# Kernel tuning notes

Hardware: AMD Instinct MI355X
Metric: run time of the kernel (lower is better)

## Reference

```python
import jax, jax.numpy as jnp
import numpy as np

N_RAYS = 65536
N_COARSE = 64
N_FINE = 128


def setup_inputs() -> dict:
    key = jax.random.key(0)
    k0, k1, k2 = jax.random.split(key, 3)
    origins = jax.random.normal(k0, (N_RAYS, 3), dtype=jnp.float32)
    directions = jax.random.normal(k1, (N_RAYS, 3), dtype=jnp.float32)
    near = jnp.full((N_RAYS,), 2.0, dtype=jnp.float32)
    far = jnp.full((N_RAYS,), 6.0, dtype=jnp.float32)
    # coarse-pass weights used for inverse-CDF (PDF) fine sampling
    weights = jax.random.uniform(k2, (N_RAYS, N_COARSE), dtype=jnp.float32)
    return {"origins": origins, "directions": directions, "near": near,
            "far": far, "weights": weights}


def sample_pdf(bins, weights, n_samples):
    """Inverse-CDF sampling. bins: [N, B], weights: [N, B-1] -> [N, n_samples]."""
    w = weights + 1e-5                       # avoid nans / empty bins
    pdf = w / jnp.sum(w, axis=-1, keepdims=True)
    cdf = jnp.cumsum(pdf, axis=-1)
    cdf = jnp.concatenate([jnp.zeros_like(cdf[..., :1]), cdf], axis=-1)  # [N, B]
    # deterministic (perturb=False) uniform samples in [0, 1]
    u = jnp.linspace(0.0, 1.0, n_samples, dtype=cdf.dtype)
    u = jnp.broadcast_to(u, cdf.shape[:-1] + (n_samples,))
    inds = jax.vmap(lambda c, uu: jnp.searchsorted(c, uu, side="right"))(cdf, u)
    below = jnp.clip(inds - 1, 0, cdf.shape[-1] - 1)
    above = jnp.clip(inds, 0, cdf.shape[-1] - 1)
    cdf_b = jnp.take_along_axis(cdf, below, axis=-1)
    cdf_a = jnp.take_along_axis(cdf, above, axis=-1)
    bins_b = jnp.take_along_axis(bins, below, axis=-1)
    bins_a = jnp.take_along_axis(bins, above, axis=-1)
    denom = cdf_a - cdf_b
    denom = jnp.where(denom < 1e-5, jnp.ones_like(denom), denom)
    t = (u - cdf_b) / denom
    return bins_b + t * (bins_a - bins_b)


def reference(origins, directions, near, far, weights):
    # normalize ray directions (RayBundle.__post_init__)
    directions = directions / jnp.linalg.norm(directions, axis=-1, keepdims=True)
    # stratified coarse depths (uniform in depth, perturb=False)
    t = jnp.linspace(0.0, 1.0, N_COARSE, dtype=origins.dtype)
    z_coarse = near[:, None] + (far - near)[:, None] * t          # [N, 64]
    # hierarchical PDF sampling on interval midpoints (NeRF convention)
    mids = 0.5 * (z_coarse[:, 1:] + z_coarse[:, :-1])             # [N, 63]
    z_fine = sample_pdf(mids, weights[:, 1:-1], N_FINE)           # [N, 128]
    # merge + sort by depth (RaySamples.merge / sort_by_depth)
    z = jnp.sort(jnp.concatenate([z_coarse, z_fine], axis=-1), axis=-1)  # [N, 192]
    positions = origins[:, None, :] + z[..., None] * directions[:, None, :]
    view_directions = jnp.broadcast_to(directions[:, None, :], positions.shape)
    d = jnp.diff(z, axis=-1)
    deltas = jnp.concatenate([d, d[:, -1:]], axis=-1)             # last delta repeats
    return positions, view_directions, z, deltas
```

## Files before the change

kernel.cpp:

```cpp
#include <hip/hip_runtime.h>

#define NR 65536
#define RPB 4

__global__ __launch_bounds__(256) void ray_sampler_kernel(
    const float* __restrict__ origins,
    const float* __restrict__ directions,
    const float* __restrict__ nearv,
    const float* __restrict__ farv,
    const float* __restrict__ weights,
    float* __restrict__ out)
{
    __shared__ float s_cdf[RPB][64];
    __shared__ float s_coarse[RPB][64];
    __shared__ float s_fine[RPB][128];
    __shared__ float s_z[RPB][192];

    const int tid  = threadIdx.x;
    const int wv   = tid >> 6;
    const int lane = tid & 63;
    const int r    = blockIdx.x * RPB + wv;

    const float nr  = nearv[r];
    const float fr  = farv[r];
    const float dnf = fr - nr;

    float dx = directions[3*r+0];
    float dy = directions[3*r+1];
    float dz = directions[3*r+2];
    const float invn = 1.0f / sqrtf(dx*dx + dy*dy + dz*dz);
    dx *= invn; dy *= invn; dz *= invn;
    const float ox = origins[3*r+0];
    const float oy = origins[3*r+1];
    const float oz = origins[3*r+2];

    float w = 0.0f;
    if (lane < 62) w = weights[(size_t)r*64 + lane + 1] + 1e-5f;
    float sc = w;
    #pragma unroll
    for (int off = 1; off < 64; off <<= 1) {
        float t = __shfl_up(sc, off, 64);
        if (lane >= off) sc += t;
    }
    const float total = __shfl(sc, 63, 64);
    const float invT  = 1.0f / total;
    if (lane < 62) s_cdf[wv][lane + 1] = sc * invT;
    if (lane == 62) s_cdf[wv][0] = 0.0f;

    s_coarse[wv][lane] = nr + dnf * ((float)lane * (1.0f/63.0f));
    __syncthreads();

    const float* cdf = s_cdf[wv];
    #pragma unroll
    for (int sIt = 0; sIt < 2; ++sIt) {
        const int s = lane + sIt * 64;
        const float u = (float)s * (1.0f/127.0f);
        int lo = 0, hi = 63;
        #pragma unroll
        for (int it = 0; it < 6; ++it) {
            if (lo < hi) {
                int mid = (lo + hi) >> 1;
                if (cdf[mid] <= u) lo = mid + 1; else hi = mid;
            }
        }
        int below = lo - 1; below = below < 0 ? 0 : (below > 62 ? 62 : below);
        int above = lo > 62 ? 62 : lo;
        const float cb = cdf[below], ca = cdf[above];
        const float bb = nr + dnf * (((float)below + 0.5f) * (1.0f/63.0f));
        const float ba = nr + dnf * (((float)above + 0.5f) * (1.0f/63.0f));
        float den = ca - cb;
        if (den < 1e-5f) den = 1.0f;
        const float tt = (u - cb) / den;
        s_fine[wv][s] = bb + tt * (ba - bb);
    }
    __syncthreads();

    const float* fine   = s_fine[wv];
    const float* coarse = s_coarse[wv];
    {
        const float v = coarse[lane];
        int lo = 0, hi = 128;
        #pragma unroll
        for (int it = 0; it < 8; ++it) {
            if (lo < hi) {
                int mid = (lo + hi) >> 1;
                if (fine[mid] < v) lo = mid + 1; else hi = mid;
            }
        }
        s_z[wv][lane + lo] = v;
    }
    #pragma unroll
    for (int sIt = 0; sIt < 2; ++sIt) {
        const int s = lane + sIt * 64;
        const float v = fine[s];
        int lo = 0, hi = 64;
        #pragma unroll
        for (int it = 0; it < 7; ++it) {
            if (lo < hi) {
                int mid = (lo + hi) >> 1;
                if (coarse[mid] <= v) lo = mid + 1; else hi = mid;
            }
        }
        s_z[wv][s + lo] = v;
    }
    __syncthreads();

    const float* zm = s_z[wv];
    float4* pos4 = reinterpret_cast<float4*>(out) + (size_t)r * 144;
    float4* vd4  = reinterpret_cast<float4*>(out + (size_t)NR * 576)  + (size_t)r * 144;
    float4* z4   = reinterpret_cast<float4*>(out + (size_t)NR * 1152) + (size_t)r * 48;
    float4* dl4  = reinterpret_cast<float4*>(out + (size_t)NR * 1344) + (size_t)r * 48;

    #pragma unroll
    for (int qi = 0; qi < 3; ++qi) {
        const int q = lane + qi * 64;
        if (q < 144) {
            const int f = 4 * q;
            float4 p, v;
            #pragma unroll
            for (int m = 0; m < 4; ++m) {
                const int k = (f + m) / 3;
                const int c = (f + m) % 3;
                const float zz = zm[k];
                const float dc = (c == 0) ? dx : ((c == 1) ? dy : dz);
                const float oc = (c == 0) ? ox : ((c == 1) ? oy : oz);
                (&p.x)[m] = oc + zz * dc;
                (&v.x)[m] = dc;
            }
            pos4[q] = p;
            vd4[q]  = v;
        }
    }
    if (lane < 48) {
        const int f = 4 * lane;
        const float z0 = zm[f], z1 = zm[f+1], z2 = zm[f+2], z3 = zm[f+3];
        z4[lane] = make_float4(z0, z1, z2, z3);
        const bool hasNext = (f + 4) < 192;
        const float e3 = hasNext ? (zm[f+4] - z3) : (z3 - z2);
        dl4[lane] = make_float4(z1 - z0, z2 - z1, z3 - z2, e3);
    }
}

extern "C" void kernel_launch(void* const* d_in, const int* in_sizes, int n_in,
                              void* d_out, int out_size, void* d_ws, size_t ws_size,
                              hipStream_t stream) {
    const float* origins    = (const float*)d_in[0];
    const float* directions = (const float*)d_in[1];
    const float* nearv      = (const float*)d_in[2];
    const float* farv       = (const float*)d_in[3];
    const float* weights    = (const float*)d_in[4];
    float* out = (float*)d_out;

    dim3 grid(NR / RPB);
    dim3 block(256);
    ray_sampler_kernel<<<grid, block, 0, stream>>>(origins, directions, nearv, farv, weights, out);
}
```

Before: 83.54 us.

## Drop block barriers, stage positions in LDS, use nontemporal coalesced stores

Removes every __syncthreads, since each wavefront owns one ray and touches only its own LDS rows. Coarse depths are now computed analytically instead of being read from shared memory. Positions are staged in LDS so each lane writes whole float4 vectors, and view directions come from a small precomputed 12-float pattern. All output writes use nontemporal stores to lighten cache pressure on a write-bound kernel. Dropping the barriers relies on wavefront lockstep execution for cross-lane LDS visibility, with no explicit fence, which is a correctness risk.

```diff
diff --git a/kernel.cpp b/kernel.cpp
--- a/kernel.cpp
+++ b/kernel.cpp
@@ -2,6 +2,12 @@
 
 #define NR 65536
 #define RPB 4
+
+typedef float f32x4 __attribute__((ext_vector_type(4)));
+
+__device__ __forceinline__ float coarse_at(int j, float nr, float dnf) {
+    return fmaf((float)j * (1.0f / 63.0f), dnf, nr);
+}
 
 __global__ __launch_bounds__(256) void ray_sampler_kernel(
     const float* __restrict__ origins,
@@ -12,9 +18,10 @@
     float* __restrict__ out)
 {
     __shared__ float s_cdf[RPB][64];
-    __shared__ float s_coarse[RPB][64];
     __shared__ float s_fine[RPB][128];
     __shared__ float s_z[RPB][192];
+    __shared__ float s_pos[RPB][576];
+    __shared__ float s_vd[RPB][16];
 
     const int tid  = threadIdx.x;
     const int wv   = tid >> 6;
@@ -34,6 +41,11 @@
     const float oy = origins[3*r+1];
     const float oz = origins[3*r+2];
 
+    if (lane < 12) {
+        const int c = lane % 3;
+        s_vd[wv][lane] = (c == 0) ? dx : ((c == 1) ? dy : dz);
+    }
+
     float w = 0.0f;
     if (lane < 62) w = weights[(size_t)r*64 + lane + 1] + 1e-5f;
     float sc = w;
@@ -47,10 +59,8 @@
     if (lane < 62) s_cdf[wv][lane + 1] = sc * invT;
     if (lane == 62) s_cdf[wv][0] = 0.0f;
 
-    s_coarse[wv][lane] = nr + dnf * ((float)lane * (1.0f/63.0f));
-    __syncthreads();
-
     const float* cdf = s_cdf[wv];
+    float fval0, fval1;
     #pragma unroll
     for (int sIt = 0; sIt < 2; ++sIt) {
         const int s = lane + sIt * 64;
@@ -66,19 +76,19 @@
         int below = lo - 1; below = below < 0 ? 0 : (below > 62 ? 62 : below);
         int above = lo > 62 ? 62 : lo;
         const float cb = cdf[below], ca = cdf[above];
-        const float bb = nr + dnf * (((float)below + 0.5f) * (1.0f/63.0f));
-        const float ba = nr + dnf * (((float)above + 0.5f) * (1.0f/63.0f));
+        const float bb = fmaf(((float)below + 0.5f) * (1.0f/63.0f), dnf, nr);
+        const float ba = fmaf(((float)above + 0.5f) * (1.0f/63.0f), dnf, nr);
         float den = ca - cb;
         if (den < 1e-5f) den = 1.0f;
         const float tt = (u - cb) / den;
-        s_fine[wv][s] = bb + tt * (ba - bb);
+        const float fv = bb + tt * (ba - bb);
+        s_fine[wv][s] = fv;
+        if (sIt == 0) fval0 = fv; else fval1 = fv;
     }
-    __syncthreads();
 
-    const float* fine   = s_fine[wv];
-    const float* coarse = s_coarse[wv];
+    const float* fine = s_fine[wv];
     {
-        const float v = coarse[lane];
+        const float v = coarse_at(lane, nr, dnf);
         int lo = 0, hi = 128;
         #pragma unroll
         for (int it = 0; it < 8; ++it) {
@@ -91,53 +101,55 @@
     }
     #pragma unroll
     for (int sIt = 0; sIt < 2; ++sIt) {
-        const int s = lane + sIt * 64;
-        const float v = fine[s];
+        const float v = (sIt == 0) ? fval0 : fval1;
         int lo = 0, hi = 64;
         #pragma unroll
         for (int it = 0; it < 7; ++it) {
             if (lo < hi) {
                 int mid = (lo + hi) >> 1;
-                if (coarse[mid] <= v) lo = mid + 1; else hi = mid;
+                if (coarse_at(mid, nr, dnf) <= v) lo = mid + 1; else hi = mid;
             }
         }
-        s_z[wv][s + lo] = v;
+        s_z[wv][lane + sIt * 64 + lo] = v;
     }
-    __syncthreads();
 
     const float* zm = s_z[wv];
-    float4* pos4 = reinterpret_cast<float4*>(out) + (size_t)r * 144;
-    float4* vd4  = reinterpret_cast<float4*>(out + (size_t)NR * 576)  + (size_t)r * 144;
-    float4* z4   = reinterpret_cast<float4*>(out + (size_t)NR * 1152) + (size_t)r * 48;
-    float4* dl4  = reinterpret_cast<float4*>(out + (size_t)NR * 1344) + (size_t)r * 48;
+    float* posb = out + (size_t)r * 576;
+    float* vdb  = out + (size_t)NR * 576  + (size_t)r * 576;
+    float* zb   = out + (size_t)NR * 1152 + (size_t)r * 192;
+    float* dlb  = out + (size_t)NR * 1344 + (size_t)r * 192;
 
     #pragma unroll
-    for (int qi = 0; qi < 3; ++qi) {
+    for (int ri = 0; ri < 3; ++ri) {
+        const int k  = lane + ri * 64;
+        const float zz = zm[k];
+        const int kn = (k == 191) ? 190 : (k + 1);
+        const float zn = zm[kn];
+        const float dl = fabsf(zn - zz);
+        s_pos[wv][3*k + 0] = fmaf(zz, dx, ox);
+        s_pos[wv][3*k + 1] = fmaf(zz, dy, oy);
+        s_pos[wv][3*k + 2] = fmaf(zz, dz, oz);
+        __builtin_nontemporal_store(zz, zb + k);
+        __builtin_nontemporal_store(dl, dlb + k);
+    }
+
+    int l3 = lane % 3;
+    const f32x4* posp = reinterpret_cast<const f32x4*>(s_pos[wv]);
+    const f32x4* vdp  = reinterpret_cast<const f32x4*>(s_vd[wv]);
+    f32x4* pos4 = reinterpret_cast<f32x4*>(posb);
+    f32x4* vd4  = reinterpret_cast<f32x4*>(vdb);
+    #pragma unroll
+    for (int qi = 0; qi < 2; ++qi) {
         const int q = lane + qi * 64;
-        if (q < 144) {
-            const int f = 4 * q;
-            float4 p, v;
-            #pragma unroll
-            for (int m = 0; m < 4; ++m) {
-                const int k = (f + m) / 3;
-                const int c = (f + m) % 3;
-                const float zz = zm[k];
-                const float dc = (c == 0) ? dx : ((c == 1) ? dy : dz);
-                const float oc = (c == 0) ? ox : ((c == 1) ? oy : oz);
-                (&p.x)[m] = oc + zz * dc;
-                (&v.x)[m] = dc;
-            }
-            pos4[q] = p;
-            vd4[q]  = v;
-        }
+        int p = l3 + qi; p -= (p >= 3) ? 3 : 0;
+        __builtin_nontemporal_store(posp[q], pos4 + q);
+        __builtin_nontemporal_store(vdp[p],  vd4 + q);
     }
-    if (lane < 48) {
-        const int f = 4 * lane;
-        const float z0 = zm[f], z1 = zm[f+1], z2 = zm[f+2], z3 = zm[f+3];
-        z4[lane] = make_float4(z0, z1, z2, z3);
-        const bool hasNext = (f + 4) < 192;
-        const float e3 = hasNext ? (zm[f+4] - z3) : (z3 - z2);
-        dl4[lane] = make_float4(z1 - z0, z2 - z1, z3 - z2, e3);
+    if (lane < 16) {
+        const int q = 128 + lane;
+        int p = l3 + 2; p -= (p >= 3) ? 3 : 0;
+        __builtin_nontemporal_store(posp[q], pos4 + q);
+        __builtin_nontemporal_store(vdp[p],  vd4 + q);
     }
 }
 
```

Result: faster. 81.56 us (-2.4%).
